# Performance work log

Measured on AMD Instinct MI355X. Metric: run time of the kernel, lower is better.

Reference implementation:

```python
import jax, jax.numpy as jnp
import numpy as np

WS = 7
B, Dd, Hh, Wd, C, NH = 1, 28, 28, 28, 384, 12

def _rel_index(ws):
    coords = np.stack(np.meshgrid(np.arange(ws), np.arange(ws), np.arange(ws), indexing='ij'))
    cf = coords.reshape(3, -1)
    rel = (cf[:, :, None] - cf[:, None, :]).transpose(1, 2, 0) + (ws - 1)
    rel[:, :, 0] *= (2 * ws - 1) ** 2
    rel[:, :, 1] *= (2 * ws - 1)
    return rel.sum(-1)  # (ws^3, ws^3)

REL_IDX = _rel_index(WS)

def setup_inputs():
    key = jax.random.key(0)
    ks = jax.random.split(key, 8)
    L = Dd * Hh * Wd
    s = 0.02
    return {
        'skip': jax.random.normal(ks[0], (B, L, C), jnp.float32),
        'x_up': jax.random.normal(ks[1], (B, L, C), jnp.float32),
        'D': Dd, 'H': Hh, 'W': Wd,
        'ln1_g': jnp.ones((C,), jnp.float32), 'ln1_b': jnp.zeros((C,), jnp.float32),
        'kv_w': jax.random.normal(ks[2], (C, 2 * C), jnp.float32) * s,
        'kv_b': jnp.zeros((2 * C,), jnp.float32),
        'rpb': jax.random.normal(ks[3], ((2 * WS - 1) ** 3, NH), jnp.float32) * s,
        'proj_w': jax.random.normal(ks[4], (C, C), jnp.float32) * s,
        'proj_b': jnp.zeros((C,), jnp.float32),
        'ln2_g': jnp.ones((C,), jnp.float32), 'ln2_b': jnp.zeros((C,), jnp.float32),
        'mlp_w1': jax.random.normal(ks[5], (C, 4 * C), jnp.float32) * s,
        'mlp_b1': jnp.zeros((4 * C,), jnp.float32),
        'mlp_w2': jax.random.normal(ks[6], (4 * C, C), jnp.float32) * s,
        'mlp_b2': jnp.zeros((C,), jnp.float32),
    }

def _ln(x, g, b):
    m = jnp.mean(x, -1, keepdims=True)
    v = jnp.mean(jnp.square(x - m), -1, keepdims=True)
    return (x - m) * jax.lax.rsqrt(v + 1e-5) * g + b

def _win_part(x):
    b, d, h, w, c = x.shape
    x = x.reshape(b, d // WS, WS, h // WS, WS, w // WS, WS, c)
    return x.transpose(0, 1, 3, 5, 2, 4, 6, 7).reshape(-1, WS ** 3, c)

def _win_rev(x, b, d, h, w):
    c = x.shape[-1]
    x = x.reshape(b, d // WS, h // WS, w // WS, WS, WS, WS, c)
    return x.transpose(0, 1, 4, 2, 5, 3, 6, 7).reshape(b, d, h, w, c)

def reference(skip, x_up, D, H, W, ln1_g, ln1_b, kv_w, kv_b, rpb, proj_w, proj_b, ln2_g, ln2_b, mlp_w1, mlp_b1, mlp_w2, mlp_b2):
    b, L, c = skip.shape
    x = x_up + skip  # wrapper residual; shortcut of the inner block
    # inner block was built with shift_size=0 -> no cyclic shift, attn_mask unused
    sk = _win_part(_ln(skip, ln1_g, ln1_b).reshape(b, D, H, W, c))   # (nW, N, C) -> K,V source
    qx = _win_part(_ln(x_up, ln1_g, ln1_b).reshape(b, D, H, W, c))   # (nW, N, C) -> Q source
    nW, N, _ = sk.shape
    hd = c // NH
    kv = (sk @ kv_w + kv_b).reshape(nW, N, 2, NH, hd)
    k, v = kv[:, :, 0], kv[:, :, 1]                  # (nW, N, NH, hd)
    q = qx.reshape(nW, N, NH, hd) * (hd ** -0.5)     # no q projection in WindowAttention_kv
    attn = jnp.einsum('wqhd,wkhd->whqk', q, k)
    bias = rpb[REL_IDX.reshape(-1)].reshape(N, N, NH).transpose(2, 0, 1)
    attn = jax.nn.softmax(attn + bias[None], axis=-1)
    o = jnp.einsum('whqk,wkhd->wqhd', attn, v).reshape(nW, N, c)
    o = o @ proj_w + proj_b
    o = _win_rev(o, b, D, H, W).reshape(b, L, c)
    x = x + o
    h1 = jax.nn.gelu(_ln(x, ln2_g, ln2_b) @ mlp_w1 + mlp_b1)
    x = x + h1 @ mlp_w2 + mlp_b2
    return x
```

## Files before the change

kernel.cpp:

```cpp
#include <hip/hip_runtime.h>
#include <hip/hip_bf16.h>
#include <cstdint>

typedef unsigned short u16;
typedef short s16x8 __attribute__((ext_vector_type(8)));
typedef float f32x4 __attribute__((ext_vector_type(4)));

#define C_DIM 384
#define NHEAD 12
#define HD    32
#define NTOK  343
#define NWIN  64
#define LTOT  21952
#define SIDE  28

__device__ __forceinline__ float u2f(u16 u) {
    return __uint_as_float(((unsigned int)u) << 16);
}
__device__ __forceinline__ u16 f2b(float f) {
    unsigned int u = __float_as_uint(f);
    return (u16)((u + 0x7fffu + ((u >> 16) & 1u)) >> 16);
}
__device__ __forceinline__ float gelu_tanh(float x) {
    float x3 = x * x * x;
    return 0.5f * x * (1.f + tanhf(0.7978845608028654f * (x + 0.044715f * x3)));
}

__global__ __launch_bounds__(256) void k_wt(
    const float* __restrict__ W, u16* __restrict__ Wt, int K, int N)
{
    __shared__ float T[64][65];
    int k0 = blockIdx.x * 64, n0 = blockIdx.y * 64;
    int t = threadIdx.x;
    int c = t & 63, rg = t >> 6;
#pragma unroll
    for (int i = 0; i < 16; i++) {
        int r = rg * 16 + i;
        T[r][c] = W[(size_t)(k0 + r) * N + n0 + c];
    }
    __syncthreads();
    int k = t & 63, ng = t >> 6;
#pragma unroll
    for (int i = 0; i < 16; i++) {
        int n = ng * 16 + i;
        Wt[(size_t)(n0 + n) * K + k0 + k] = f2b(T[k][n]);
    }
}

__global__ __launch_bounds__(256) void k_lnprep(
    const float* __restrict__ skip, const float* __restrict__ xup,
    const float* __restrict__ g, const float* __restrict__ bta,
    u16* __restrict__ skW, u16* __restrict__ qW)
{
    int t = blockIdx.x * 4 + (threadIdx.x >> 6);
    int lane = threadIdx.x & 63;
    const float* ps = skip + (size_t)t * C_DIM;
    const float* px = xup + (size_t)t * C_DIM;
    float vs[6], vx[6];
    float s1 = 0.f, s2 = 0.f, x1 = 0.f, x2 = 0.f;
#pragma unroll
    for (int j = 0; j < 6; j++) {
        float a = ps[lane + j * 64];
        float b = px[lane + j * 64];
        vs[j] = a; vx[j] = b;
        s1 += a; s2 += a * a; x1 += b; x2 += b * b;
    }
#pragma unroll
    for (int off = 32; off; off >>= 1) {
        s1 += __shfl_xor(s1, off);
        s2 += __shfl_xor(s2, off);
        x1 += __shfl_xor(x1, off);
        x2 += __shfl_xor(x2, off);
    }
    float ms = s1 * (1.f / 384.f), mx = x1 * (1.f / 384.f);
    float rs = rsqrtf(fmaxf(s2 * (1.f / 384.f) - ms * ms, 0.f) + 1e-5f);
    float rx = rsqrtf(fmaxf(x2 * (1.f / 384.f) - mx * mx, 0.f) + 1e-5f);
    int d = t / 784, rem = t % 784, hh = rem / 28, ww = rem % 28;
    int win = (d / 7) * 16 + (hh / 7) * 4 + (ww / 7);
    int n = (d % 7) * 49 + (hh % 7) * 7 + (ww % 7);
    size_t dst = ((size_t)(win * NTOK + n)) * C_DIM + lane;
#pragma unroll
    for (int j = 0; j < 6; j++) {
        int c = lane + j * 64;
        float gg = g[c], bb = bta[c];
        skW[dst + j * 64] = f2b((vs[j] - ms) * rs * gg + bb);
        qW[dst + j * 64]  = f2b((vx[j] - mx) * rx * gg + bb);
    }
}

__global__ __launch_bounds__(256) void k_ln2(
    const u16* __restrict__ x2, const float* __restrict__ g,
    const float* __restrict__ bta, u16* __restrict__ lnx)
{
    int t = blockIdx.x * 4 + (threadIdx.x >> 6);
    int lane = threadIdx.x & 63;
    const u16* p = x2 + (size_t)t * C_DIM;
    float v[6];
    float s1 = 0.f, s2 = 0.f;
#pragma unroll
    for (int j = 0; j < 6; j++) {
        float a = u2f(p[lane + j * 64]);
        v[j] = a; s1 += a; s2 += a * a;
    }
#pragma unroll
    for (int off = 32; off; off >>= 1) {
        s1 += __shfl_xor(s1, off);
        s2 += __shfl_xor(s2, off);
    }
    float m = s1 * (1.f / 384.f);
    float r = rsqrtf(fmaxf(s2 * (1.f / 384.f) - m * m, 0.f) + 1e-5f);
    size_t dst = (size_t)t * C_DIM + lane;
#pragma unroll
    for (int j = 0; j < 6; j++) {
        int c = lane + j * 64;
        lnx[dst + j * 64] = f2b((v[j] - m) * r * g[c] + bta[c]);
    }
}

#define LDSW 56

__device__ __forceinline__ void gemm_mfma(
    const u16* __restrict__ A, const u16* __restrict__ Bt, int K,
    int rowBase, int colBase, int tid,
    u16 (*As)[LDSW], u16 (*Bs)[LDSW], f32x4 acc[4])
{
    const int srow = tid >> 2;
    const int scg  = tid & 3;
    const int lane = tid & 63, wv = tid >> 6;
    const int m16 = lane & 15, quad = lane >> 4;

    uint4 a = *(const uint4*)(A + (size_t)(rowBase + srow) * K + scg * 8);
    uint4 b = *(const uint4*)(Bt + (size_t)(colBase + srow) * K + scg * 8);

    for (int kk = 0; kk < K; kk += 32) {
        *(uint4*)&As[srow][scg * 8] = a;
        *(uint4*)&Bs[srow][scg * 8] = b;
        __syncthreads();
        if (kk + 32 < K) {
            a = *(const uint4*)(A + (size_t)(rowBase + srow) * K + kk + 32 + scg * 8);
            b = *(const uint4*)(Bt + (size_t)(colBase + srow) * K + kk + 32 + scg * 8);
        }
        s16x8 af = *(const s16x8*)&As[wv * 16 + m16][quad * 8];
#pragma unroll
        for (int nb = 0; nb < 4; nb++) {
            s16x8 bf = *(const s16x8*)&Bs[nb * 16 + m16][quad * 8];
            acc[nb] = __builtin_amdgcn_mfma_f32_16x16x32_bf16(af, bf, acc[nb], 0, 0, 0);
        }
        __syncthreads();
    }
}

#define EPI_SETUP \
    int lane = tid & 63, wv = tid >> 6, quad = lane >> 4, n16 = lane & 15;

__global__ __launch_bounds__(256) void k_gemm_kv(
    const u16* __restrict__ A, const u16* __restrict__ Wt, const float* __restrict__ bias,
    u16* __restrict__ Kb, u16* __restrict__ Vb)
{
    __shared__ __align__(16) u16 As[64][LDSW];
    __shared__ __align__(16) u16 Bs[64][LDSW];
    f32x4 acc[4] = {};
    int tid = threadIdx.x;
    int rowBase = blockIdx.x * 64, colBase = blockIdx.y * 64;
    gemm_mfma(A, Wt, 384, rowBase, colBase, tid, As, Bs, acc);
    EPI_SETUP
#pragma unroll
    for (int nb = 0; nb < 4; nb++) {
        int col = colBase + nb * 16 + n16;
        float bcol = bias[col];
        int isv = col >= 384;
        int remc = col - (isv ? 384 : 0);
        int hh = remc >> 5, dd = remc & 31;
#pragma unroll
        for (int reg = 0; reg < 4; reg++) {
            int r = rowBase + wv * 16 + quad * 4 + reg;
            int w = r / NTOK, nn = r % NTOK;
            size_t dst = ((size_t)((w * NHEAD + hh) * NTOK + nn)) * HD + dd;
            (isv ? Vb : Kb)[dst] = f2b(acc[nb][reg] + bcol);
        }
    }
}

__global__ __launch_bounds__(256) void k_gemm_proj(
    const u16* __restrict__ A, const u16* __restrict__ Wt, const float* __restrict__ bias,
    const float* __restrict__ skip, const float* __restrict__ xup, u16* __restrict__ x2)
{
    __shared__ __align__(16) u16 As[64][LDSW];
    __shared__ __align__(16) u16 Bs[64][LDSW];
    f32x4 acc[4] = {};
    int tid = threadIdx.x;
    int rowBase = blockIdx.x * 64, colBase = blockIdx.y * 64;
    gemm_mfma(A, Wt, 384, rowBase, colBase, tid, As, Bs, acc);
    EPI_SETUP
#pragma unroll
    for (int nb = 0; nb < 4; nb++) {
        int col = colBase + nb * 16 + n16;
        float bcol = bias[col];
#pragma unroll
        for (int reg = 0; reg < 4; reg++) {
            size_t r = rowBase + wv * 16 + quad * 4 + reg;
            size_t idx = r * C_DIM + col;
            x2[idx] = f2b(acc[nb][reg] + bcol + skip[idx] + xup[idx]);
        }
    }
}

__global__ __launch_bounds__(256) void k_gemm_mlp1(
    const u16* __restrict__ A, const u16* __restrict__ Wt, const float* __restrict__ bias,
    u16* __restrict__ h1c, int rowOfs)
{
    __shared__ __align__(16) u16 As[64][LDSW];
    __shared__ __align__(16) u16 Bs[64][LDSW];
    f32x4 acc[4] = {};
    int tid = threadIdx.x;
    int rowBase = rowOfs + blockIdx.x * 64, colBase = blockIdx.y * 64;
    gemm_mfma(A, Wt, 384, rowBase, colBase, tid, As, Bs, acc);
    EPI_SETUP
#pragma unroll
    for (int nb = 0; nb < 4; nb++) {
        int col = colBase + nb * 16 + n16;
        float bcol = bias[col];
#pragma unroll
        for (int reg = 0; reg < 4; reg++) {
            size_t rl = (size_t)(rowBase - rowOfs) + wv * 16 + quad * 4 + reg;
            h1c[rl * 1536 + col] = f2b(gelu_tanh(acc[nb][reg] + bcol));
        }
    }
}

__global__ __launch_bounds__(256) void k_gemm_mlp2(
    const u16* __restrict__ A, const u16* __restrict__ Wt, const float* __restrict__ bias,
    const u16* __restrict__ x2, float* __restrict__ out, int rowOfs)
{
    __shared__ __align__(16) u16 As[64][LDSW];
    __shared__ __align__(16) u16 Bs[64][LDSW];
    f32x4 acc[4] = {};
    int tid = threadIdx.x;
    int rowBase = blockIdx.x * 64, colBase = blockIdx.y * 64;
    gemm_mfma(A, Wt, 1536, rowBase, colBase, tid, As, Bs, acc);
    EPI_SETUP
#pragma unroll
    for (int nb = 0; nb < 4; nb++) {
        int col = colBase + nb * 16 + n16;
        float bcol = bias[col];
#pragma unroll
        for (int reg = 0; reg < 4; reg++) {
            size_t rg = (size_t)rowOfs + rowBase + wv * 16 + quad * 4 + reg;
            size_t idx = rg * C_DIM + col;
            out[idx] = acc[nb][reg] + bcol + u2f(x2[idx]);
        }
    }
}

#define KP 40
#define VP 360

__global__ __launch_bounds__(256, 2) void k_attn(
    const u16* __restrict__ qW, const u16* __restrict__ Kb, const u16* __restrict__ Vb,
    const float* __restrict__ rpb, u16* __restrict__ oT)
{
    __shared__ __align__(16) u16 Ks[352 * KP];
    __shared__ __align__(16) u16 Vt[32 * VP];
    __shared__ __align__(16) u16 rp16[2208];
    __shared__ __align__(16) u16 code[352];
    __shared__ __align__(16) u16 Pb[4 * 16 * KP];

    const int h = blockIdx.x, w = blockIdx.y, half = blockIdx.z;
    const int tid = threadIdx.x;
    const int lane = tid & 63, wv = tid >> 6;
    const int m16 = lane & 15, quad = lane >> 4;
    const size_t base = ((size_t)(w * NHEAD + h)) * NTOK * HD;

    for (int t = tid; t < 1408; t += 256) {
        int r = t >> 2, c = (t & 3) << 3;
        uint4 u = make_uint4(0, 0, 0, 0);
        if (r < NTOK) u = *(const uint4*)(Kb + base + r * HD + c);
        *(uint4*)&Ks[r * KP + c] = u;
    }
    for (int t = tid; t < 1408; t += 256) {
        int dg = t / 352, n = t - dg * 352;
        uint4 u = make_uint4(0, 0, 0, 0);
        if (n < NTOK) u = *(const uint4*)(Vb + base + n * HD + dg * 8);
        int d0 = dg * 8;
        Vt[(d0 + 0) * VP + n] = (u16)(u.x & 0xffff);
        Vt[(d0 + 1) * VP + n] = (u16)(u.x >> 16);
        Vt[(d0 + 2) * VP + n] = (u16)(u.y & 0xffff);
        Vt[(d0 + 3) * VP + n] = (u16)(u.y >> 16);
        Vt[(d0 + 4) * VP + n] = (u16)(u.z & 0xffff);
        Vt[(d0 + 5) * VP + n] = (u16)(u.z >> 16);
        Vt[(d0 + 6) * VP + n] = (u16)(u.w & 0xffff);
        Vt[(d0 + 7) * VP + n] = (u16)(u.w >> 16);
    }
    for (int t = tid; t < 2208; t += 256)
        rp16[t] = (t < 2197) ? f2b(rpb[t * NHEAD + h]) : (u16)0;
    for (int t = tid; t < 352; t += 256) {
        int z = t / 49, rem = t % 49, y = rem / 7, x = rem % 7;
        code[t] = (t < NTOK) ? (u16)(z * 169 + y * 13 + x) : (u16)1098;
    }
    __syncthreads();

    const float scale = 0.17677669529663687f;
    u16* myP = Pb + wv * 16 * KP;

    for (int qt = half * 11 + wv; qt < half * 11 + 11; qt += 4) {
        int qbase = qt * 16;
        int qrow = min(qbase + m16, NTOK - 1);
        s16x8 qf = *(const s16x8*)(qW + ((size_t)(w * NTOK + qrow)) * C_DIM
                                       + h * HD + quad * 8);
        int qcv[4];
#pragma unroll
        for (int i = 0; i < 4; i++) qcv[i] = code[qbase + quad * 4 + i];

        f32x4 S0[11], S1[11];
        float mx[4] = {-1e30f, -1e30f, -1e30f, -1e30f};

#pragma unroll
        for (int ks = 0; ks < 11; ks++) {
            int kbase = ks * 32;
            int kt0 = kbase + m16, kt1 = kt0 + 16;
            s16x8 kf0 = *(const s16x8*)&Ks[kt0 * KP + quad * 8];
            s16x8 kf1 = *(const s16x8*)&Ks[kt1 * KP + quad * 8];
            f32x4 z = {0.f, 0.f, 0.f, 0.f};
            f32x4 sA = __builtin_amdgcn_mfma_f32_16x16x32_bf16(qf, kf0, z, 0, 0, 0);
            f32x4 sB = __builtin_amdgcn_mfma_f32_16x16x32_bf16(qf, kf1, z, 0, 0, 0);
            int kc0 = code[kt0], kc1 = code[kt1];
            bool k1ok = (ks < 10) || (kt1 < NTOK);
#pragma unroll
            for (int i = 0; i < 4; i++) {
                float b0 = u2f(rp16[qcv[i] - kc0 + 1098]);
                float b1 = u2f(rp16[qcv[i] - kc1 + 1098]);
                float sa = fmaf(sA[i], scale, b0);
                float sb = k1ok ? fmaf(sB[i], scale, b1) : -1e30f;
                S0[ks][i] = sa;
                S1[ks][i] = sb;
                mx[i] = fmaxf(mx[i], fmaxf(sa, sb));
            }
        }
#pragma unroll
        for (int i = 0; i < 4; i++) {
            float v = mx[i];
            v = fmaxf(v, __shfl_xor(v, 1));
            v = fmaxf(v, __shfl_xor(v, 2));
            v = fmaxf(v, __shfl_xor(v, 4));
            v = fmaxf(v, __shfl_xor(v, 8));
            mx[i] = v;
        }

        f32x4 O0 = {}, O1 = {};
        float l[4] = {};
#pragma unroll
        for (int ks = 0; ks < 11; ks++) {
            int kbase = ks * 32;
#pragma unroll
            for (int i = 0; i < 4; i++) {
                float pa = __expf(S0[ks][i] - mx[i]);
                float pb = __expf(S1[ks][i] - mx[i]);
                l[i] += pa + pb;
                int prow = quad * 4 + i;
                myP[prow * KP + m16]      = f2b(pa);
                myP[prow * KP + 16 + m16] = f2b(pb);
            }
            s16x8 pf  = *(const s16x8*)&myP[m16 * KP + quad * 8];
            s16x8 vf0 = *(const s16x8*)&Vt[m16 * VP + kbase + quad * 8];
            s16x8 vf1 = *(const s16x8*)&Vt[(16 + m16) * VP + kbase + quad * 8];
            O0 = __builtin_amdgcn_mfma_f32_16x16x32_bf16(pf, vf0, O0, 0, 0, 0);
            O1 = __builtin_amdgcn_mfma_f32_16x16x32_bf16(pf, vf1, O1, 0, 0, 0);
        }
#pragma unroll
        for (int i = 0; i < 4; i++) {
            float v = l[i];
            v += __shfl_xor(v, 1);
            v += __shfl_xor(v, 2);
            v += __shfl_xor(v, 4);
            v += __shfl_xor(v, 8);
            l[i] = v;
        }

        int wd = w >> 4, wh = (w >> 2) & 3, wwi = w & 3;
#pragma unroll
        for (int i = 0; i < 4; i++) {
            int q = qbase + quad * 4 + i;
            if (q < NTOK) {
                float rl = 1.f / l[i];
                int qz = q / 49, qrem = q % 49, qy = qrem / 7, qx = qrem % 7;
                size_t tok = ((size_t)(wd * 7 + qz) * SIDE + (wh * 7 + qy)) * SIDE
                             + (wwi * 7 + qx);
                u16* op = oT + tok * C_DIM + h * HD;
                op[m16]      = f2b(O0[i] * rl);
                op[16 + m16] = f2b(O1[i] * rl);
            }
        }
    }
}

extern "C" void kernel_launch(void* const* d_in, const int* in_sizes, int n_in,
                              void* d_out, int out_size, void* d_ws, size_t ws_size,
                              hipStream_t stream)
{
    const float* skip = (const float*)d_in[0];
    const float* xup  = (const float*)d_in[1];
    const float* ln1g = (const float*)d_in[5];
    const float* ln1b = (const float*)d_in[6];
    const float* kvw  = (const float*)d_in[7];
    const float* kvb  = (const float*)d_in[8];
    const float* rpb  = (const float*)d_in[9];
    const float* pw   = (const float*)d_in[10];
    const float* pb   = (const float*)d_in[11];
    const float* ln2g = (const float*)d_in[12];
    const float* ln2b = (const float*)d_in[13];
    const float* w1   = (const float*)d_in[14];
    const float* b1   = (const float*)d_in[15];
    const float* w2   = (const float*)d_in[16];
    const float* b2   = (const float*)d_in[17];
    float* out = (float*)d_out;

    char* ws = (char*)d_ws;
    const size_t BUFB = (size_t)LTOT * C_DIM * 2;
    const size_t WTB  = 589824 + 294912 + 1179648 + 1179648;
    u16* skW = (u16*)(ws);
    u16* qW  = (u16*)(ws + BUFB);
    u16* Kb  = (u16*)(ws + 2 * BUFB);
    u16* Vb  = (u16*)(ws + 3 * BUFB);
    u16* oT  = (u16*)(ws);
    u16* x2  = (u16*)(ws + BUFB);
    u16* lnx = (u16*)(ws + 2 * BUFB);
    char* wt = ws + 4 * BUFB;
    u16* kvWt = (u16*)(wt);
    u16* pWt  = (u16*)(wt + 589824);
    u16* w1t  = (u16*)(wt + 589824 + 294912);
    u16* w2t  = (u16*)(wt + 589824 + 294912 + 1179648);

    const size_t used = 4 * BUFB + WTB;
    const size_t blkBytes = 64 * 1536 * 2;
    int chunkBlocks = 49;
    u16* h1c = (u16*)(ws + 3 * BUFB);
    if (ws_size > used) {
        int cap = (int)((ws_size - used) / blkBytes);
        if (cap >= 49) {
            chunkBlocks = cap < 343 ? cap : 343;
            h1c = (u16*)(ws + used);
        }
    }

    k_wt<<<dim3(6, 12), 256, 0, stream>>>(kvw, kvWt, 384, 768);
    k_wt<<<dim3(6, 6),  256, 0, stream>>>(pw,  pWt,  384, 384);
    k_wt<<<dim3(6, 24), 256, 0, stream>>>(w1,  w1t,  384, 1536);
    k_wt<<<dim3(24, 6), 256, 0, stream>>>(w2,  w2t,  1536, 384);

    k_lnprep<<<LTOT / 4, 256, 0, stream>>>(skip, xup, ln1g, ln1b, skW, qW);
    k_gemm_kv<<<dim3(343, 12), 256, 0, stream>>>(skW, kvWt, kvb, Kb, Vb);
    k_attn<<<dim3(NHEAD, NWIN, 2), 256, 0, stream>>>(qW, Kb, Vb, rpb, oT);
    k_gemm_proj<<<dim3(343, 6), 256, 0, stream>>>(oT, pWt, pb, skip, xup, x2);
    k_ln2<<<LTOT / 4, 256, 0, stream>>>(x2, ln2g, ln2b, lnx);
    for (int b0 = 0; b0 < 343; b0 += chunkBlocks) {
        int nb = (343 - b0) < chunkBlocks ? (343 - b0) : chunkBlocks;
        int rowOfs = b0 * 64;
        k_gemm_mlp1<<<dim3(nb, 24), 256, 0, stream>>>(lnx, w1t, b1, h1c, rowOfs);
        k_gemm_mlp2<<<dim3(nb, 6), 256, 0, stream>>>(h1c, w2t, b2, x2, out, rowOfs);
    }
}
```

Before: 475.2 us.

## Enlarge GEMM tiles to 128x128 and precompute residual sum in LN prep

All four MFMA GEMMs move from 64x64 to 128x128 output tiles, with each wave computing a 32x128 block. This raises reuse of the A and B fragments loaded into LDS and halves the grid sizes, and needs row bounds checks because 21952 is not a multiple of 128. LN prep also writes skip+x_up as a bf16 residual into the output buffer, so the projection epilogue reads one bf16 value instead of two fp32 values. GELU is rewritten as x*sigmoid(2z) using __expf instead of tanhf. The tradeoffs are higher register use per thread and bf16 rounding of the residual.

```diff
diff --git a/kernel.cpp b/kernel.cpp
--- a/kernel.cpp
+++ b/kernel.cpp
@@ -21,9 +21,9 @@
     unsigned int u = __float_as_uint(f);
     return (u16)((u + 0x7fffu + ((u >> 16) & 1u)) >> 16);
 }
-__device__ __forceinline__ float gelu_tanh(float x) {
-    float x3 = x * x * x;
-    return 0.5f * x * (1.f + tanhf(0.7978845608028654f * (x + 0.044715f * x3)));
+__device__ __forceinline__ float gelu_fast(float x) {
+    float z = 0.7978845608028654f * (x + 0.044715f * x * x * x);
+    return x / (1.f + __expf(-2.f * z));
 }
 
 __global__ __launch_bounds__(256) void k_wt(
@@ -50,7 +50,7 @@
 __global__ __launch_bounds__(256) void k_lnprep(
     const float* __restrict__ skip, const float* __restrict__ xup,
     const float* __restrict__ g, const float* __restrict__ bta,
-    u16* __restrict__ skW, u16* __restrict__ qW)
+    u16* __restrict__ skW, u16* __restrict__ qW, u16* __restrict__ res)
 {
     int t = blockIdx.x * 4 + (threadIdx.x >> 6);
     int lane = threadIdx.x & 63;
@@ -79,12 +79,14 @@
     int win = (d / 7) * 16 + (hh / 7) * 4 + (ww / 7);
     int n = (d % 7) * 49 + (hh % 7) * 7 + (ww % 7);
     size_t dst = ((size_t)(win * NTOK + n)) * C_DIM + lane;
+    size_t td  = (size_t)t * C_DIM + lane;
 #pragma unroll
     for (int j = 0; j < 6; j++) {
         int c = lane + j * 64;
         float gg = g[c], bb = bta[c];
         skW[dst + j * 64] = f2b((vs[j] - ms) * rs * gg + bb);
         qW[dst + j * 64]  = f2b((vx[j] - mx) * rx * gg + bb);
+        res[td + j * 64]  = f2b(vs[j] + vx[j]);
     }
 }
 
@@ -117,34 +119,47 @@
     }
 }
 
-#define LDSW 56
-
-__device__ __forceinline__ void gemm_mfma(
-    const u16* __restrict__ A, const u16* __restrict__ Bt, int K,
+#define BPAD 40
+
+__device__ __forceinline__ void gemm128(
+    const u16* __restrict__ A, const u16* __restrict__ Bt, int K, int M,
     int rowBase, int colBase, int tid,
-    u16 (*As)[LDSW], u16 (*Bs)[LDSW], f32x4 acc[4])
-{
-    const int srow = tid >> 2;
-    const int scg  = tid & 3;
+    u16 (*As)[BPAD], u16 (*Bs)[BPAD], f32x4 acc[2][8])
+{
+    const int sr  = tid >> 2;
+    const int scg = (tid & 3) << 3;
     const int lane = tid & 63, wv = tid >> 6;
     const int m16 = lane & 15, quad = lane >> 4;
 
-    uint4 a = *(const uint4*)(A + (size_t)(rowBase + srow) * K + scg * 8);
-    uint4 b = *(const uint4*)(Bt + (size_t)(colBase + srow) * K + scg * 8);
+    int ra0 = min(rowBase + sr, M - 1);
+    int ra1 = min(rowBase + 64 + sr, M - 1);
+    const u16* pa0 = A + (size_t)ra0 * K + scg;
+    const u16* pa1 = A + (size_t)ra1 * K + scg;
+    const u16* pb0 = Bt + (size_t)(colBase + sr) * K + scg;
+    const u16* pb1 = Bt + (size_t)(colBase + 64 + sr) * K + scg;
+
+    uint4 a0 = *(const uint4*)pa0, a1 = *(const uint4*)pa1;
+    uint4 b0 = *(const uint4*)pb0, b1 = *(const uint4*)pb1;
 
     for (int kk = 0; kk < K; kk += 32) {
-        *(uint4*)&As[srow][scg * 8] = a;
-        *(uint4*)&Bs[srow][scg * 8] = b;
+        *(uint4*)&As[sr][scg]      = a0;
+        *(uint4*)&As[64 + sr][scg] = a1;
+        *(uint4*)&Bs[sr][scg]      = b0;
+        *(uint4*)&Bs[64 + sr][scg] = b1;
         __syncthreads();
         if (kk + 32 < K) {
-            a = *(const uint4*)(A + (size_t)(rowBase + srow) * K + kk + 32 + scg * 8);
-            b = *(const uint4*)(Bt + (size_t)(colBase + srow) * K + kk + 32 + scg * 8);
-        }
-        s16x8 af = *(const s16x8*)&As[wv * 16 + m16][quad * 8];
-#pragma unroll
-        for (int nb = 0; nb < 4; nb++) {
-            s16x8 bf = *(const s16x8*)&Bs[nb * 16 + m16][quad * 8];
-            acc[nb] = __builtin_amdgcn_mfma_f32_16x16x32_bf16(af, bf, acc[nb], 0, 0, 0);
+            a0 = *(const uint4*)(pa0 + kk + 32);
+            a1 = *(const uint4*)(pa1 + kk + 32);
+            b0 = *(const uint4*)(pb0 + kk + 32);
+            b1 = *(const uint4*)(pb1 + kk + 32);
+        }
+        s16x8 af0 = *(const s16x8*)&As[wv * 32 + m16][quad * 8];
+        s16x8 af1 = *(const s16x8*)&As[wv * 32 + 16 + m16][quad * 8];
+#pragma unroll
+        for (int c = 0; c < 8; c++) {
+            s16x8 bf = *(const s16x8*)&Bs[c * 16 + m16][quad * 8];
+            acc[0][c] = __builtin_amdgcn_mfma_f32_16x16x32_bf16(af0, bf, acc[0][c], 0, 0, 0);
+            acc[1][c] = __builtin_amdgcn_mfma_f32_16x16x32_bf16(af1, bf, acc[1][c], 0, 0, 0);
         }
         __syncthreads();
     }
@@ -157,50 +172,58 @@
     const u16* __restrict__ A, const u16* __restrict__ Wt, const float* __restrict__ bias,
     u16* __restrict__ Kb, u16* __restrict__ Vb)
 {
-    __shared__ __align__(16) u16 As[64][LDSW];
-    __shared__ __align__(16) u16 Bs[64][LDSW];
-    f32x4 acc[4] = {};
+    __shared__ __align__(16) u16 As[128][BPAD];
+    __shared__ __align__(16) u16 Bs[128][BPAD];
+    f32x4 acc[2][8] = {};
     int tid = threadIdx.x;
-    int rowBase = blockIdx.x * 64, colBase = blockIdx.y * 64;
-    gemm_mfma(A, Wt, 384, rowBase, colBase, tid, As, Bs, acc);
+    int rowBase = blockIdx.x * 128, colBase = blockIdx.y * 128;
+    gemm128(A, Wt, 384, LTOT, rowBase, colBase, tid, As, Bs, acc);
     EPI_SETUP
 #pragma unroll
-    for (int nb = 0; nb < 4; nb++) {
-        int col = colBase + nb * 16 + n16;
+    for (int c = 0; c < 8; c++) {
+        int col = colBase + c * 16 + n16;
         float bcol = bias[col];
         int isv = col >= 384;
         int remc = col - (isv ? 384 : 0);
         int hh = remc >> 5, dd = remc & 31;
 #pragma unroll
+        for (int rt = 0; rt < 2; rt++)
+#pragma unroll
         for (int reg = 0; reg < 4; reg++) {
-            int r = rowBase + wv * 16 + quad * 4 + reg;
-            int w = r / NTOK, nn = r % NTOK;
-            size_t dst = ((size_t)((w * NHEAD + hh) * NTOK + nn)) * HD + dd;
-            (isv ? Vb : Kb)[dst] = f2b(acc[nb][reg] + bcol);
+            int r = rowBase + wv * 32 + rt * 16 + quad * 4 + reg;
+            if (r < LTOT) {
+                int w = r / NTOK, nn = r % NTOK;
+                size_t dst = ((size_t)((w * NHEAD + hh) * NTOK + nn)) * HD + dd;
+                (isv ? Vb : Kb)[dst] = f2b(acc[rt][c][reg] + bcol);
+            }
         }
     }
 }
 
 __global__ __launch_bounds__(256) void k_gemm_proj(
     const u16* __restrict__ A, const u16* __restrict__ Wt, const float* __restrict__ bias,
-    const float* __restrict__ skip, const float* __restrict__ xup, u16* __restrict__ x2)
-{
-    __shared__ __align__(16) u16 As[64][LDSW];
-    __shared__ __align__(16) u16 Bs[64][LDSW];
-    f32x4 acc[4] = {};
+    const u16* __restrict__ res, u16* __restrict__ x2)
+{
+    __shared__ __align__(16) u16 As[128][BPAD];
+    __shared__ __align__(16) u16 Bs[128][BPAD];
+    f32x4 acc[2][8] = {};
     int tid = threadIdx.x;
-    int rowBase = blockIdx.x * 64, colBase = blockIdx.y * 64;
-    gemm_mfma(A, Wt, 384, rowBase, colBase, tid, As, Bs, acc);
+    int rowBase = blockIdx.x * 128, colBase = blockIdx.y * 128;
+    gemm128(A, Wt, 384, LTOT, rowBase, colBase, tid, As, Bs, acc);
     EPI_SETUP
 #pragma unroll
-    for (int nb = 0; nb < 4; nb++) {
-        int col = colBase + nb * 16 + n16;
+    for (int c = 0; c < 8; c++) {
+        int col = colBase + c * 16 + n16;
         float bcol = bias[col];
 #pragma unroll
+        for (int rt = 0; rt < 2; rt++)
+#pragma unroll
         for (int reg = 0; reg < 4; reg++) {
-            size_t r = rowBase + wv * 16 + quad * 4 + reg;
-            size_t idx = r * C_DIM + col;
-            x2[idx] = f2b(acc[nb][reg] + bcol + skip[idx] + xup[idx]);
+            int r = rowBase + wv * 32 + rt * 16 + quad * 4 + reg;
+            if (r < LTOT) {
+                size_t idx = (size_t)r * C_DIM + col;
+                x2[idx] = f2b(acc[rt][c][reg] + bcol + u2f(res[idx]));
+            }
         }
     }
 }
@@ -209,45 +232,55 @@
     const u16* __restrict__ A, const u16* __restrict__ Wt, const float* __restrict__ bias,
     u16* __restrict__ h1c, int rowOfs)
 {
-    __shared__ __align__(16) u16 As[64][LDSW];
-    __shared__ __align__(16) u16 Bs[64][LDSW];
-    f32x4 acc[4] = {};
+    __shared__ __align__(16) u16 As[128][BPAD];
+    __shared__ __align__(16) u16 Bs[128][BPAD];
+    f32x4 acc[2][8] = {};
     int tid = threadIdx.x;
-    int rowBase = rowOfs + blockIdx.x * 64, colBase = blockIdx.y * 64;
-    gemm_mfma(A, Wt, 384, rowBase, colBase, tid, As, Bs, acc);
+    int rowBase = rowOfs + blockIdx.x * 128, colBase = blockIdx.y * 128;
+    gemm128(A, Wt, 384, LTOT, rowBase, colBase, tid, As, Bs, acc);
     EPI_SETUP
 #pragma unroll
-    for (int nb = 0; nb < 4; nb++) {
-        int col = colBase + nb * 16 + n16;
+    for (int c = 0; c < 8; c++) {
+        int col = colBase + c * 16 + n16;
         float bcol = bias[col];
 #pragma unroll
+        for (int rt = 0; rt < 2; rt++)
+#pragma unroll
         for (int reg = 0; reg < 4; reg++) {
-            size_t rl = (size_t)(rowBase - rowOfs) + wv * 16 + quad * 4 + reg;
-            h1c[rl * 1536 + col] = f2b(gelu_tanh(acc[nb][reg] + bcol));
+            int r = rowBase + wv * 32 + rt * 16 + quad * 4 + reg;
+            if (r < LTOT) {
+                size_t rl = (size_t)(r - rowOfs);
+                h1c[rl * 1536 + col] = f2b(gelu_fast(acc[rt][c][reg] + bcol));
+            }
         }
     }
 }
 
 __global__ __launch_bounds__(256) void k_gemm_mlp2(
     const u16* __restrict__ A, const u16* __restrict__ Wt, const float* __restrict__ bias,
-    const u16* __restrict__ x2, float* __restrict__ out, int rowOfs)
-{
-    __shared__ __align__(16) u16 As[64][LDSW];
-    __shared__ __align__(16) u16 Bs[64][LDSW];
-    f32x4 acc[4] = {};
+    const u16* __restrict__ x2, float* __restrict__ out, int rowOfs, int chunkRows)
+{
+    __shared__ __align__(16) u16 As[128][BPAD];
+    __shared__ __align__(16) u16 Bs[128][BPAD];
+    f32x4 acc[2][8] = {};
     int tid = threadIdx.x;
-    int rowBase = blockIdx.x * 64, colBase = blockIdx.y * 64;
-    gemm_mfma(A, Wt, 1536, rowBase, colBase, tid, As, Bs, acc);
+    int rowBase = blockIdx.x * 128, colBase = blockIdx.y * 128;
+    gemm128(A, Wt, 1536, chunkRows, rowBase, colBase, tid, As, Bs, acc);
     EPI_SETUP
 #pragma unroll
-    for (int nb = 0; nb < 4; nb++) {
-        int col = colBase + nb * 16 + n16;
+    for (int c = 0; c < 8; c++) {
+        int col = colBase + c * 16 + n16;
         float bcol = bias[col];
 #pragma unroll
+        for (int rt = 0; rt < 2; rt++)
+#pragma unroll
         for (int reg = 0; reg < 4; reg++) {
-            size_t rg = (size_t)rowOfs + rowBase + wv * 16 + quad * 4 + reg;
-            size_t idx = rg * C_DIM + col;
-            out[idx] = acc[nb][reg] + bcol + u2f(x2[idx]);
+            int rl = rowBase + wv * 32 + rt * 16 + quad * 4 + reg;
+            int rg = rowOfs + rl;
+            if (rl < chunkRows && rg < LTOT) {
+                size_t idx = (size_t)rg * C_DIM + col;
+                out[idx] = acc[rt][c][reg] + bcol + u2f(x2[idx]);
+            }
         }
     }
 }
@@ -429,17 +462,19 @@
     u16* pWt  = (u16*)(wt + 589824);
     u16* w1t  = (u16*)(wt + 589824 + 294912);
     u16* w2t  = (u16*)(wt + 589824 + 294912 + 1179648);
+    u16* res  = (u16*)d_out;
 
     const size_t used = 4 * BUFB + WTB;
-    const size_t blkBytes = 64 * 1536 * 2;
-    int chunkBlocks = 49;
-    u16* h1c = (u16*)(ws + 3 * BUFB);
-    if (ws_size > used) {
-        int cap = (int)((ws_size - used) / blkBytes);
-        if (cap >= 49) {
-            chunkBlocks = cap < 343 ? cap : 343;
-            h1c = (u16*)(ws + used);
-        }
+    const size_t blkBytes = 128 * 1536 * 2;
+    size_t tailCap = (ws_size > used) ? (ws_size - used) / blkBytes : 0;
+    int chunkBlocks;
+    u16* h1c;
+    if (tailCap >= 43) {
+        chunkBlocks = tailCap < 172 ? (int)tailCap : 172;
+        h1c = (u16*)(ws + used);
+    } else {
+        chunkBlocks = 42;
+        h1c = (u16*)(ws + 3 * BUFB);
     }
 
     k_wt<<<dim3(6, 12), 256, 0, stream>>>(kvw, kvWt, 384, 768);
@@ -447,15 +482,17 @@
     k_wt<<<dim3(6, 24), 256, 0, stream>>>(w1,  w1t,  384, 1536);
     k_wt<<<dim3(24, 6), 256, 0, stream>>>(w2,  w2t,  1536, 384);
 
-    k_lnprep<<<LTOT / 4, 256, 0, stream>>>(skip, xup, ln1g, ln1b, skW, qW);
-    k_gemm_kv<<<dim3(343, 12), 256, 0, stream>>>(skW, kvWt, kvb, Kb, Vb);
+    k_lnprep<<<LTOT / 4, 256, 0, stream>>>(skip, xup, ln1g, ln1b, skW, qW, res);
+    k_gemm_kv<<<dim3(172, 6), 256, 0, stream>>>(skW, kvWt, kvb, Kb, Vb);
     k_attn<<<dim3(NHEAD, NWIN, 2), 256, 0, stream>>>(qW, Kb, Vb, rpb, oT);
-    k_gemm_proj<<<dim3(343, 6), 256, 0, stream>>>(oT, pWt, pb, skip, xup, x2);
+    k_gemm_proj<<<dim3(172, 3), 256, 0, stream>>>(oT, pWt, pb, res, x2);
     k_ln2<<<LTOT / 4, 256, 0, stream>>>(x2, ln2g, ln2b, lnx);
-    for (int b0 = 0; b0 < 343; b0 += chunkBlocks) {
-        int nb = (343 - b0) < chunkBlocks ? (343 - b0) : chunkBlocks;
-        int rowOfs = b0 * 64;
-        k_gemm_mlp1<<<dim3(nb, 24), 256, 0, stream>>>(lnx, w1t, b1, h1c, rowOfs);
-        k_gemm_mlp2<<<dim3(nb, 6), 256, 0, stream>>>(h1c, w2t, b2, x2, out, rowOfs);
-    }
-}
+    for (int b0 = 0; b0 < 172; b0 += chunkBlocks) {
+        int nb = (172 - b0) < chunkBlocks ? (172 - b0) : chunkBlocks;
+        int rowOfs = b0 * 128;
+        int chunkRows = nb * 128;
+        if (rowOfs + chunkRows > LTOT) chunkRows = LTOT - rowOfs;
+        k_gemm_mlp1<<<dim3(nb, 12), 256, 0, stream>>>(lnx, w1t, b1, h1c, rowOfs);
+        k_gemm_mlp2<<<dim3(nb, 3), 256, 0, stream>>>(h1c, w2t, b2, x2, out, rowOfs, chunkRows);
+    }
+}
```

After: 473.8 us. Within noise of the previous version (-0.3%).
